# Optimization experiments

Measured on AMD Instinct MI355X. Metric: run time of the kernel, lower is better.

## Reference

```python
import jax, jax.numpy as jnp
import numpy as np

B, N, F, G, H = 8, 1024, 512, 128, 8
D = F // H  # head_dim = 64


def setup_inputs() -> dict:
    key = jax.random.key(0)
    ks = jax.random.split(key, 24)
    def lin(k, fan_in, shape):
        return jax.random.normal(k, shape, jnp.float32) / np.sqrt(fan_in)
    return {
        "features": jax.random.normal(ks[0], (B, N, F), jnp.float32),
        "geometry": jax.random.normal(ks[1], (B, N, G), jnp.float32),
        "coords": jax.random.normal(ks[2], (B, N, 3), jnp.float32),
        # nnx.MultiHeadAttention params (q/k/v/out dense, with bias)
        "wq": lin(ks[3], F, (F, F)), "bq": jnp.zeros((F,), jnp.float32),
        "wk": lin(ks[4], F, (F, F)), "bk": jnp.zeros((F,), jnp.float32),
        "wv": lin(ks[5], F, (F, F)), "bv": jnp.zeros((F,), jnp.float32),
        "wo": lin(ks[6], F, (F, F)), "bo": jnp.zeros((F,), jnp.float32),
        # geometry q/k/v linears
        "gq_w": lin(ks[7], G, (G, F)), "gq_b": jnp.zeros((F,), jnp.float32),
        "gk_w": lin(ks[8], G, (G, F)), "gk_b": jnp.zeros((F,), jnp.float32),
        "gv_w": lin(ks[9], G, (G, F)), "gv_b": jnp.zeros((F,), jnp.float32),
        # distance MLP: Linear(1->H), gelu, Linear(H->H)
        "d1_w": lin(ks[10], 1, (1, H)), "d1_b": jnp.zeros((H,), jnp.float32),
        "d2_w": lin(ks[11], H, (H, H)), "d2_b": jnp.zeros((H,), jnp.float32),
        # output projection
        "op_w": lin(ks[12], F, (F, F)), "op_b": jnp.zeros((F,), jnp.float32),
    }


def _forward(features, geometry, coords,
             wq, bq, wk, bk, wv, bv, wo, bo,
             gq_w, gq_b, gk_w, gk_b, gv_w, gv_b,
             d1_w, d1_b, d2_w, d2_b, op_w, op_b):
    scale = jnp.sqrt(jnp.float32(D))
    # --- standard multi-head self-attention branch (nnx.MultiHeadAttention) ---
    q = (features @ wq + bq).reshape(B, N, H, D)
    k = (features @ wk + bk).reshape(B, N, H, D)
    v = (features @ wv + bv).reshape(B, N, H, D)
    scores = jnp.einsum("bqhd,bkhd->bhqk", q, k) / scale
    attn = jax.nn.softmax(scores, axis=-1)
    feat_att = jnp.einsum("bhqk,bkhd->bqhd", attn, v).reshape(B, N, F)
    feat_att = feat_att @ wo + bo
    # --- geometry attention branch ---
    gq = geometry @ gq_w + gq_b
    gk = geometry @ gk_w + gk_b
    gv = geometry @ gv_w + gv_b
    g_scores = jnp.einsum("bqd,bkd->bqk", gq, gk) / scale
    # pairwise distances (B,N,N,1); clamp for sqrt-at-zero safety (diagonal)
    diff = coords[:, :, None, :] - coords[:, None, :, :]
    dist = jnp.sqrt(jnp.maximum(jnp.sum(diff * diff, -1, keepdims=True), 1e-12))
    dw = jax.nn.gelu(dist @ d1_w + d1_b) @ d2_w + d2_b  # (B,N,N,H)
    # transpose to (B,H,N,N) then mean over heads == mean over last axis
    g_scores = g_scores + jnp.mean(dw, axis=-1)
    g_attn = jax.nn.softmax(g_scores, axis=-1)
    geom_att = jnp.einsum("bqk,bkd->bqd", g_attn, gv)
    return (feat_att + geom_att) @ op_w + op_b


def reference(features, geometry, coords,
              wq, bq, wk, bk, wv, bv, wo, bo,
              gq_w, gq_b, gk_w, gk_b, gv_w, gv_b,
              d1_w, d1_b, d2_w, d2_b, op_w, op_b):
    return _forward(features, geometry, coords,
                    wq, bq, wk, bk, wv, bv, wo, bo,
                    gq_w, gq_b, gk_w, gk_b, gv_w, gv_b,
                    d1_w, d1_b, d2_w, d2_b, op_w, op_b)
```

## Files before the change

kernel.cpp:

```cpp
#include <hip/hip_runtime.h>

typedef __bf16 bf16_t;
typedef __bf16 bf16x8 __attribute__((ext_vector_type(8)));
typedef __bf16 bf16x4v __attribute__((ext_vector_type(4)));
typedef float f32x4 __attribute__((ext_vector_type(4)));

#define MFMA16(a, b, c) __builtin_amdgcn_mfma_f32_16x16x32_bf16((a), (b), (c), 0, 0, 0)

static constexpr int B_ = 8, N_ = 1024, F_ = 512, H_ = 8;
static constexpr int M_ = B_ * N_;

__device__ __forceinline__ void gl_lds16(const bf16_t* gsrc, bf16_t* ldst) {
  __builtin_amdgcn_global_load_lds(
      (const __attribute__((address_space(1))) void*)gsrc,
      (__attribute__((address_space(3))) void*)ldst, 16, 0, 0);
}

__device__ __forceinline__ float gelu_tanh(float u) {
  float g = 0.7978845608028654f * fmaf(0.044715f * u * u, u, u);
  float e = __expf(2.f * g);
  float t = 1.f - 2.f / (e + 1.f);
  return 0.5f * u * (1.f + t);
}

struct PrepArgs {
  const float *features, *geometry;
  const float *wq, *wk, *wv, *wo, *op_w;
  const float *gq_w, *gk_w, *gv_w;
  const float *bq, *bk, *bv, *gq_b, *gk_b, *gv_b;
  const float *d1w, *d1b, *d2w, *d2b;
  bf16_t *featBF, *geomBF, *WqkvT, *GqkvT, *WoT, *OpT;
  float *bqkv, *gqkvb, *dlut;
};

static constexpr int PR_C0 = 4096;
static constexpr int PR_C1 = PR_C0 + 1024;
static constexpr int PR_WQ = PR_C1 + 256;
static constexpr int PR_WK = PR_WQ + 256;
static constexpr int PR_WV = PR_WK + 256;
static constexpr int PR_WO = PR_WV + 256;
static constexpr int PR_OP = PR_WO + 256;
static constexpr int PR_GQ = PR_OP + 64;
static constexpr int PR_GK = PR_GQ + 64;
static constexpr int PR_GV = PR_GK + 64;
static constexpr int PR_B1 = PR_GV + 6;
static constexpr int PR_B2 = PR_B1 + 6;
static constexpr int PR_LUT = PR_B2 + 16;
static constexpr int PR_TOTAL = PR_LUT;

__device__ __forceinline__ void prep_cast(const float* __restrict__ in,
                                          bf16_t* __restrict__ out, int blk) {
  int i = blk * 256 + threadIdx.x;
  float4 v = ((const float4*)in)[i];
  bf16x4v o;
  o[0] = (bf16_t)v.x; o[1] = (bf16_t)v.y; o[2] = (bf16_t)v.z; o[3] = (bf16_t)v.w;
  ((bf16x4v*)out)[i] = o;
}

__device__ __forceinline__ void prep_transpose(const float* __restrict__ W,
                                               bf16_t* __restrict__ Wt,
                                               int K, int N, int ldo, int idx,
                                               float (*t)[33]) {
  const int bx = idx & 15, by = idx >> 4;
  const int kb = by * 32, cb = bx * 32;
  const int tx = threadIdx.x & 31, ty = threadIdx.x >> 5;
#pragma unroll
  for (int i = 0; i < 4; ++i)
    t[ty * 4 + i][tx] = W[(long)(kb + ty * 4 + i) * N + cb + tx];
  __syncthreads();
#pragma unroll
  for (int i = 0; i < 4; ++i)
    Wt[(long)(cb + ty * 4 + i) * ldo + kb + tx] = (bf16_t)t[tx][ty * 4 + i];
}

__global__ __launch_bounds__(256) void k_prep(PrepArgs p) {
  __shared__ float tsh[32][33];
  const int blk = blockIdx.x;
  if (blk < PR_C0) {
    prep_cast(p.features, p.featBF, blk);
  } else if (blk < PR_C1) {
    prep_cast(p.geometry, p.geomBF, blk - PR_C0);
  } else if (blk < PR_WQ) {
    prep_transpose(p.wq, p.WqkvT, 512, 512, 512, blk - PR_C1, tsh);
  } else if (blk < PR_WK) {
    prep_transpose(p.wk, p.WqkvT + 512 * 512, 512, 512, 512, blk - PR_WQ, tsh);
  } else if (blk < PR_WV) {
    prep_transpose(p.wv, p.WqkvT + 1024 * 512, 512, 512, 512, blk - PR_WK, tsh);
  } else if (blk < PR_WO) {
    prep_transpose(p.wo, p.WoT, 512, 512, 512, blk - PR_WV, tsh);
  } else if (blk < PR_OP) {
    prep_transpose(p.op_w, p.OpT, 512, 512, 512, blk - PR_WO, tsh);
  } else if (blk < PR_GQ) {
    prep_transpose(p.gq_w, p.GqkvT, 128, 512, 128, blk - PR_OP, tsh);
  } else if (blk < PR_GK) {
    prep_transpose(p.gk_w, p.GqkvT + 512 * 128, 128, 512, 128, blk - PR_GQ, tsh);
  } else if (blk < PR_GV) {
    prep_transpose(p.gv_w, p.GqkvT + 1024 * 128, 128, 512, 128, blk - PR_GK, tsh);
  } else if (blk < PR_B1) {
    int i = (blk - PR_GV) * 256 + threadIdx.x;
    p.bqkv[i] = i < 512 ? p.bq[i] : (i < 1024 ? p.bk[i - 512] : p.bv[i - 1024]);
  } else if (blk < PR_B2) {
    int i = (blk - PR_B1) * 256 + threadIdx.x;
    p.gqkvb[i] = i < 512 ? p.gq_b[i] : (i < 1024 ? p.gk_b[i - 512] : p.gv_b[i - 1024]);
  } else {
    int i = (blk - PR_B2) * 256 + threadIdx.x;
    float d = (i + 0.5f) * (16.f / 4096.f);
    float s = 0.f;
#pragma unroll
    for (int h = 0; h < 8; ++h) s += p.d2b[h];
    s *= 0.125f;
#pragma unroll
    for (int j = 0; j < 8; ++j) {
      float w2 = 0.f;
#pragma unroll
      for (int h = 0; h < 8; ++h) w2 += p.d2w[j * 8 + h];
      s = fmaf(gelu_tanh(fmaf(d, p.d1w[j], p.d1b[j])), w2 * 0.125f, s);
    }
    p.dlut[i] = s;
  }
}

__global__ void k_transpose_v2(const bf16_t* __restrict__ QKV,
                               const bf16_t* __restrict__ GQKV,
                               bf16_t* __restrict__ Vt, bf16_t* __restrict__ GVt) {
  __shared__ bf16_t t[32][33];
  const int z = blockIdx.z;
  const bf16_t* in = z < 8 ? QKV : GQKV;
  bf16_t* out = z < 8 ? Vt : GVt;
  const int b = z & 7;
  const int cb = blockIdx.x * 32, nb = blockIdx.y * 32;
  const int tx = threadIdx.x, ty = threadIdx.y;
#pragma unroll
  for (int i = 0; i < 4; ++i)
    t[ty * 4 + i][tx] = in[((long)b * 1024 + nb + ty * 4 + i) * 1536 + 1024 + cb + tx];
  __syncthreads();
#pragma unroll
  for (int i = 0; i < 4; ++i)
    out[((long)b * 512 + cb + ty * 4 + i) * 1024 + nb + tx] = t[tx][ty * 4 + i];
}

struct GemmArgs {
  const bf16_t* A; const bf16_t* Bt;
  const float* bias; const float* addSrc;
  const float* coords; const float* lut;
  float* outF; bf16_t* outB;
  long strideAb; long strideBb;
  int lda, ldb, K, ldout;
  float scale;
};

__device__ __forceinline__ void gemm128_core(const GemmArgs& g, int mBase, int cBase,
                                             bf16_t (*As)[64], bf16_t (*Bs)[64]) {
  const int tid = threadIdx.x;
  const int w = tid >> 6, lane = tid & 63;
  const int lr = lane & 15, lg = lane >> 4;
  const int wr = w >> 1, wc = w & 1;
  const int batch = mBase >> 10;

  const int srow = lane >> 3;
  const int scol = (lane & 7) * 8;
  const bf16_t* Ag = g.A + (long)batch * g.strideAb +
                     (long)((mBase & 1023) + w * 32 + srow) * g.lda + scol;
  const bf16_t* Bg = g.Bt + (long)batch * g.strideBb +
                     (long)(cBase + w * 32 + srow) * g.ldb + scol;
  bf16_t* Al = &As[w * 32][0];
  bf16_t* Bl = &Bs[w * 32][0];

  f32x4 zero = {0.f, 0.f, 0.f, 0.f};
  f32x4 acc[4][4];
#pragma unroll
  for (int i = 0; i < 4; ++i)
#pragma unroll
    for (int j = 0; j < 4; ++j) acc[i][j] = zero;

  for (int k0 = 0; k0 < g.K; k0 += 64) {
#pragma unroll
    for (int is = 0; is < 4; ++is) {
      gl_lds16(Ag + (long)(is * 8) * g.lda + k0, Al + is * 8 * 64);
      gl_lds16(Bg + (long)(is * 8) * g.ldb + k0, Bl + is * 8 * 64);
    }
    __syncthreads();
#pragma unroll
    for (int ks = 0; ks < 2; ++ks) {
      bf16x8 a[4], b[4];
#pragma unroll
      for (int i = 0; i < 4; ++i) {
        a[i] = *(const bf16x8*)(&As[wr * 64 + i * 16 + lr][ks * 32 + lg * 8]);
        b[i] = *(const bf16x8*)(&Bs[wc * 64 + i * 16 + lr][ks * 32 + lg * 8]);
      }
#pragma unroll
      for (int mf = 0; mf < 4; ++mf)
#pragma unroll
        for (int nf = 0; nf < 4; ++nf)
          acc[mf][nf] = MFMA16(a[mf], b[nf], acc[mf][nf]);
    }
    __syncthreads();
  }

  const int c0 = cBase + wc * 64;
  float bias4[4];
#pragma unroll
  for (int nf = 0; nf < 4; ++nf)
    bias4[nf] = g.bias ? g.bias[c0 + nf * 16 + lr] : 0.f;
#pragma unroll
  for (int mf = 0; mf < 4; ++mf) {
    const int r0 = mBase + wr * 64 + mf * 16 + lg * 4;
#pragma unroll
    for (int nf = 0; nf < 4; ++nf) {
      const int c = c0 + nf * 16 + lr;
#pragma unroll
      for (int rg = 0; rg < 4; ++rg) {
        const int r = r0 + rg;
        float v = acc[mf][nf][rg] * g.scale + bias4[nf];
        if (g.addSrc) v += g.addSrc[(long)r * g.ldout + c];
        const long oi = (long)r * g.ldout + c;
        if (g.outF) g.outF[oi] = v;
        if (g.outB) g.outB[oi] = (bf16_t)v;
      }
    }
  }
}

__global__ __launch_bounds__(256) void k_gemm128_dual(GemmArgs g1, GemmArgs g2) {
  __shared__ alignas(16) bf16_t As[128][64];
  __shared__ alignas(16) bf16_t Bs[128][64];
  const int y = blockIdx.y;
  if (y < 64) gemm128_core(g1, y * 128, blockIdx.x * 128, As, Bs);
  else        gemm128_core(g2, (y - 64) * 128, blockIdx.x * 128, As, Bs);
}

__device__ __forceinline__ void gemm128_dist(const GemmArgs& g, int mBase, int cBase,
                                             char* smemc) {
  bf16_t (*As)[64] = (bf16_t (*)[64])smemc;
  bf16_t (*Bs)[64] = (bf16_t (*)[64])(smemc + 16384);
  bf16_t* Lut = (bf16_t*)(smemc + 32768);
  const int tid = threadIdx.x;
  const int w = tid >> 6, lane = tid & 63;
  const int lr = lane & 15, lg = lane >> 4;
  const int wr = w >> 1, wc = w & 1;
  const int batch = mBase >> 10;

  {
    const float4* src = (const float4*)g.lut;
#pragma unroll
    for (int i = 0; i < 4; ++i) {
      float4 v = src[tid + i * 256];
      bf16x4v o;
      o[0] = (bf16_t)v.x; o[1] = (bf16_t)v.y; o[2] = (bf16_t)v.z; o[3] = (bf16_t)v.w;
      ((bf16x4v*)Lut)[tid + i * 256] = o;
    }
  }

  const int srow = lane >> 3;
  const int scol = (lane & 7) * 8;
  const bf16_t* Ag = g.A + (long)batch * g.strideAb +
                     (long)((mBase & 1023) + w * 32 + srow) * g.lda + scol;
  const bf16_t* Bg = g.Bt + (long)batch * g.strideBb +
                     (long)(cBase + w * 32 + srow) * g.ldb + scol;
  bf16_t* Al = &As[w * 32][0];
  bf16_t* Bl = &Bs[w * 32][0];

  f32x4 zero = {0.f, 0.f, 0.f, 0.f};
  f32x4 acc[4][4];
#pragma unroll
  for (int i = 0; i < 4; ++i)
#pragma unroll
    for (int j = 0; j < 4; ++j) acc[i][j] = zero;

  for (int k0 = 0; k0 < g.K; k0 += 64) {
#pragma unroll
    for (int is = 0; is < 4; ++is) {
      gl_lds16(Ag + (long)(is * 8) * g.lda + k0, Al + is * 8 * 64);
      gl_lds16(Bg + (long)(is * 8) * g.ldb + k0, Bl + is * 8 * 64);
    }
    __syncthreads();
#pragma unroll
    for (int ks = 0; ks < 2; ++ks) {
      bf16x8 a[4], b[4];
#pragma unroll
      for (int i = 0; i < 4; ++i) {
        a[i] = *(const bf16x8*)(&As[wr * 64 + i * 16 + lr][ks * 32 + lg * 8]);
        b[i] = *(const bf16x8*)(&Bs[wc * 64 + i * 16 + lr][ks * 32 + lg * 8]);
      }
#pragma unroll
      for (int mf = 0; mf < 4; ++mf)
#pragma unroll
        for (int nf = 0; nf < 4; ++nf)
          acc[mf][nf] = MFMA16(a[mf], b[nf], acc[mf][nf]);
    }
    __syncthreads();
  }

  const int c0 = cBase + wc * 64;
  float ckx[4], cky[4], ckz[4];
#pragma unroll
  for (int nf = 0; nf < 4; ++nf) {
    const float* ck = g.coords + ((long)batch * 1024 + c0 + nf * 16 + lr) * 3;
    ckx[nf] = ck[0]; cky[nf] = ck[1]; ckz[nf] = ck[2];
  }
#pragma unroll
  for (int mf = 0; mf < 4; ++mf) {
    const int r0 = mBase + wr * 64 + mf * 16 + lg * 4;
    float cqx[4], cqy[4], cqz[4];
#pragma unroll
    for (int rg = 0; rg < 4; ++rg) {
      const float* cq = g.coords + ((long)batch * 1024 + ((r0 + rg) & 1023)) * 3;
      cqx[rg] = cq[0]; cqy[rg] = cq[1]; cqz[rg] = cq[2];
    }
#pragma unroll
    for (int nf = 0; nf < 4; ++nf) {
      const int c = c0 + nf * 16 + lr;
#pragma unroll
      for (int rg = 0; rg < 4; ++rg) {
        const int r = r0 + rg;
        float v = acc[mf][nf][rg] * g.scale;
        float dx = cqx[rg] - ckx[nf], dy = cqy[rg] - cky[nf], dz = cqz[rg] - ckz[nf];
        float d = sqrtf(fmaxf(dx * dx + dy * dy + dz * dz, 1e-12f));
        int idx = (int)(d * 256.f);
        idx = idx > 4095 ? 4095 : idx;
        v += (float)Lut[idx];
        g.outF[(long)r * g.ldout + c] = v;
      }
    }
  }
}

__device__ __forceinline__ void flash_core(const bf16_t* __restrict__ QKV,
                                           const bf16_t* __restrict__ Vt,
                                           bf16_t* __restrict__ fatt,
                                           int qx, int bh, char* smemc) {
  bf16_t (*Ks)[64][64] = (bf16_t (*)[64][64])smemc;
  bf16_t (*Vs)[64][64] = (bf16_t (*)[64][64])(smemc + 16384);
  char* Plb = smemc + 32768;
  const int wave = threadIdx.x >> 6, lane = threadIdx.x & 63;
  const int lr = lane & 15, lg = (lane >> 4) & 3;
  const int b = bh >> 3, h = bh & 7;
  const int qbase = qx * 64 + wave * 16;

  const bf16_t* Qb = QKV + (long)b * 1024 * 1536 + h * 64;
  const bf16_t* Kb = Qb + 512;
  const bf16_t* Vg = Vt + ((long)b * 512 + h * 64) * 1024;

  constexpr float SCL = 0.18033688011112042f;
  bf16x8 q_[2];
#pragma unroll
  for (int dh = 0; dh < 2; ++dh) {
    bf16x8 raw = *(const bf16x8*)(Qb + (long)(qbase + lr) * 1536 + dh * 32 + lg * 8);
#pragma unroll
    for (int j = 0; j < 8; ++j) q_[dh][j] = (bf16_t)((float)raw[j] * SCL);
  }

  const int srow = lane >> 3;
  const int scol = (((lane & 7) ^ srow) << 3);
  const bf16_t* KgB = Kb + (long)(wave * 16 + srow) * 1536 + scol;
  const bf16_t* VgB = Vg + (long)(wave * 16 + srow) * 1024 + scol;

  auto stage = [&](int buf, int kt) {
#pragma unroll
    for (int i = 0; i < 2; ++i) {
      gl_lds16(KgB + (long)(kt + i * 8) * 1536, &Ks[buf][wave * 16 + i * 8][0]);
      gl_lds16(VgB + (long)(i * 8) * 1024 + kt, &Vs[buf][wave * 16 + i * 8][0]);
    }
  };

  f32x4 zero = {0.f, 0.f, 0.f, 0.f};
  f32x4 oacc[4] = {zero, zero, zero, zero};
  float lsum0 = 0.f, lsum1 = 0.f;
  const int swz = (lr & 7) << 4;
  char* PlW = Plb + wave * 1280;

  stage(0, 0);
  asm volatile("s_waitcnt vmcnt(0)" ::: "memory");
  __syncthreads();

  auto tile = [&](const int buf, int t) __attribute__((always_inline)) {
    if (t < 15) stage(buf ^ 1, (t + 1) * 64);
    const char* KB = (const char*)&Ks[buf][0][0];
    const char* VB = (const char*)&Vs[buf][0][0];
#pragma unroll
    for (int kk = 0; kk < 2; ++kk) {
      f32x4 S[2];
      __builtin_amdgcn_s_setprio(1);
#pragma unroll
      for (int kh = 0; kh < 2; ++kh) {
        const int row = kk * 32 + kh * 16 + lr;
        bf16x8 k0 = *(const bf16x8*)(KB + row * 128 + ((lg * 16) ^ swz));
        bf16x8 k1 = *(const bf16x8*)(KB + row * 128 + ((64 + lg * 16) ^ swz));
        f32x4 tt = MFMA16(k0, q_[0], zero);
        S[kh] = MFMA16(k1, q_[1], tt);
      }
      __builtin_amdgcn_s_setprio(0);
#pragma unroll
      for (int kh = 0; kh < 2; ++kh) {
        bf16x4v pp;
#pragma unroll
        for (int r = 0; r < 4; ++r) {
          float e = exp2f(S[kh][r]);
          if (kh) lsum1 += e; else lsum0 += e;
          pp[r] = (bf16_t)e;
        }
        *(bf16x4v*)(PlW + lr * 80 + kh * 32 + lg * 8) = pp;
      }
      asm volatile("s_waitcnt lgkmcnt(0)" ::: "memory");
      const bf16x8 pa = *(const bf16x8*)(PlW + lr * 80 + lg * 16);
      __builtin_amdgcn_s_setprio(1);
#pragma unroll
      for (int ct = 0; ct < 4; ++ct) {
        const int vrow = ct * 16 + lr;
        bf16x8 vf = *(const bf16x8*)(VB + vrow * 128 + ((kk * 64 + lg * 16) ^ swz));
        oacc[ct] = MFMA16(pa, vf, oacc[ct]);
      }
      __builtin_amdgcn_s_setprio(0);
    }
    asm volatile("s_waitcnt vmcnt(0)" ::: "memory");
    __syncthreads();
  };

  for (int tt = 0; tt < 8; ++tt) {
    tile(0, tt * 2);
    tile(1, tt * 2 + 1);
  }

  float lsum = lsum0 + lsum1;
  lsum += __shfl_xor(lsum, 16);
  lsum += __shfl_xor(lsum, 32);
#pragma unroll
  for (int r = 0; r < 4; ++r) {
    float inv = 1.f / __shfl(lsum, lg * 4 + r, 64);
    int q = qbase + lg * 4 + r;
    bf16_t* orow = fatt + ((long)b * 1024 + q) * 512 + h * 64;
#pragma unroll
    for (int ct = 0; ct < 4; ++ct)
      orow[ct * 16 + lr] = (bf16_t)(oacc[ct][r] * inv);
  }
}

__global__ __launch_bounds__(256) void k_gsc_flash(GemmArgs g,
                                                   const bf16_t* __restrict__ QKV,
                                                   const bf16_t* __restrict__ Vt,
                                                   bf16_t* __restrict__ fatt) {
  __shared__ alignas(16) char smem[40960];
  const int bx = blockIdx.x;
  if (bx < 1024) {
    flash_core(QKV, Vt, fatt, bx & 15, bx >> 4, smem);
  } else {
    const int i = bx - 1024;
    gemm128_dist(g, (i >> 3) * 128, (i & 7) * 128, smem);
  }
}

__device__ __forceinline__ void gemm_n64_core(const GemmArgs& g, int mBase, int cBase,
                                              char* smemc) {
  bf16_t (*As)[64] = (bf16_t (*)[64])smemc;
  bf16_t (*Bs)[64] = (bf16_t (*)[64])(smemc + 16384);
  const int tid = threadIdx.x;
  const int w = tid >> 6, lane = tid & 63;
  const int lr = lane & 15, lg = lane >> 4;
  const int wr = w >> 1, wc = w & 1;
  const int batch = mBase >> 10;

  const int srow = lane >> 3;
  const int scol = (lane & 7) * 8;
  const bf16_t* Ag = g.A + (long)batch * g.strideAb +
                     (long)((mBase & 1023) + w * 32 + srow) * g.lda + scol;
  const bf16_t* Bg = g.Bt + (long)batch * g.strideBb +
                     (long)(cBase + w * 16 + srow) * g.ldb + scol;
  bf16_t* Al = &As[w * 32][0];
  bf16_t* Bl = &Bs[w * 16][0];

  f32x4 zero = {0.f, 0.f, 0.f, 0.f};
  f32x4 acc[4][2];
#pragma unroll
  for (int i = 0; i < 4; ++i)
#pragma unroll
    for (int j = 0; j < 2; ++j) acc[i][j] = zero;

  for (int k0 = 0; k0 < g.K; k0 += 64) {
#pragma unroll
    for (int is = 0; is < 4; ++is)
      gl_lds16(Ag + (long)(is * 8) * g.lda + k0, Al + is * 8 * 64);
#pragma unroll
    for (int is = 0; is < 2; ++is)
      gl_lds16(Bg + (long)(is * 8) * g.ldb + k0, Bl + is * 8 * 64);
    __syncthreads();
#pragma unroll
    for (int ks = 0; ks < 2; ++ks) {
      bf16x8 a[4], b[2];
#pragma unroll
      for (int i = 0; i < 4; ++i)
        a[i] = *(const bf16x8*)(&As[wr * 64 + i * 16 + lr][ks * 32 + lg * 8]);
#pragma unroll
      for (int j = 0; j < 2; ++j)
        b[j] = *(const bf16x8*)(&Bs[wc * 32 + j * 16 + lr][ks * 32 + lg * 8]);
#pragma unroll
      for (int mf = 0; mf < 4; ++mf)
#pragma unroll
        for (int nf = 0; nf < 2; ++nf)
          acc[mf][nf] = MFMA16(a[mf], b[nf], acc[mf][nf]);
    }
    __syncthreads();
  }

  const int c0 = cBase + wc * 32;
  float bias2[2];
#pragma unroll
  for (int nf = 0; nf < 2; ++nf)
    bias2[nf] = g.bias ? g.bias[c0 + nf * 16 + lr] : 0.f;
#pragma unroll
  for (int mf = 0; mf < 4; ++mf) {
    const int r0 = mBase + wr * 64 + mf * 16 + lg * 4;
#pragma unroll
    for (int nf = 0; nf < 2; ++nf) {
      const int c = c0 + nf * 16 + lr;
#pragma unroll
      for (int rg = 0; rg < 4; ++rg) {
        const int r = r0 + rg;
        float v = acc[mf][nf][rg] * g.scale + bias2[nf];
        if (g.addSrc) v += g.addSrc[(long)r * g.ldout + c];
        const long oi = (long)r * g.ldout + c;
        if (g.outF) g.outF[oi] = v;
        if (g.outB) g.outB[oi] = (bf16_t)v;
      }
    }
  }
}

__global__ __launch_bounds__(256) void k_gemm_n64(GemmArgs g) {
  __shared__ alignas(16) char smem[24576];
  gemm_n64_core(g, blockIdx.y * 128, blockIdx.x * 64, smem);
}

__device__ __forceinline__ void softmax_core(const float* __restrict__ S,
                                             bf16_t* __restrict__ P, int row,
                                             float* redM, float* redS) {
  const float* s = S + (long)row * 1024;
  const int tid = threadIdx.x;
  float4 v = ((const float4*)s)[tid];
  float mx = fmaxf(fmaxf(v.x, v.y), fmaxf(v.z, v.w));
#pragma unroll
  for (int d = 1; d < 64; d <<= 1) mx = fmaxf(mx, __shfl_xor(mx, d));
  if ((tid & 63) == 0) redM[tid >> 6] = mx;
  __syncthreads();
  mx = fmaxf(fmaxf(redM[0], redM[1]), fmaxf(redM[2], redM[3]));
  float e0 = __expf(v.x - mx), e1 = __expf(v.y - mx);
  float e2 = __expf(v.z - mx), e3 = __expf(v.w - mx);
  float sm = e0 + e1 + e2 + e3;
#pragma unroll
  for (int d = 1; d < 64; d <<= 1) sm += __shfl_xor(sm, d);
  if ((tid & 63) == 0) redS[tid >> 6] = sm;
  __syncthreads();
  sm = redS[0] + redS[1] + redS[2] + redS[3];
  float inv = 1.f / sm;
  bf16x4v o;
  o[0] = (bf16_t)(e0 * inv); o[1] = (bf16_t)(e1 * inv);
  o[2] = (bf16_t)(e2 * inv); o[3] = (bf16_t)(e3 * inv);
  ((bf16x4v*)(P + (long)row * 1024))[tid] = o;
}

__global__ __launch_bounds__(256) void k_sm_combf(GemmArgs g,
                                                  const float* __restrict__ S,
                                                  bf16_t* __restrict__ P) {
  __shared__ alignas(16) char smem[24576];
  __shared__ float redM[4], redS[4];
  const int bx = blockIdx.x;
  if (bx < 512) {
    gemm_n64_core(g, (bx >> 3) * 128, (bx & 7) * 64, smem);
  } else {
    softmax_core(S, P, bx - 512, redM, redS);
  }
}

extern "C" void kernel_launch(void* const* d_in, const int* in_sizes, int n_in,
                              void* d_out, int out_size, void* d_ws, size_t ws_size,
                              hipStream_t stream) {
  const float* features = (const float*)d_in[0];
  const float* geometry = (const float*)d_in[1];
  const float* coords   = (const float*)d_in[2];
  const float* wq = (const float*)d_in[3];  const float* bq = (const float*)d_in[4];
  const float* wk = (const float*)d_in[5];  const float* bk = (const float*)d_in[6];
  const float* wv = (const float*)d_in[7];  const float* bv = (const float*)d_in[8];
  const float* wo = (const float*)d_in[9];  const float* bo = (const float*)d_in[10];
  const float* gq_w = (const float*)d_in[11]; const float* gq_b = (const float*)d_in[12];
  const float* gk_w = (const float*)d_in[13]; const float* gk_b = (const float*)d_in[14];
  const float* gv_w = (const float*)d_in[15]; const float* gv_b = (const float*)d_in[16];
  const float* d1_w = (const float*)d_in[17]; const float* d1_b = (const float*)d_in[18];
  const float* d2_w = (const float*)d_in[19]; const float* d2_b = (const float*)d_in[20];
  const float* op_w = (const float*)d_in[21]; const float* op_b = (const float*)d_in[22];

  size_t off = 0;
  auto carve = [&](size_t bytes) {
    void* p = (char*)d_ws + off;
    off += (bytes + 255) & ~(size_t)255;
    return p;
  };
  bf16_t* featBF = (bf16_t*)carve((size_t)M_ * F_ * 2);
  bf16_t* geomBF = (bf16_t*)carve((size_t)M_ * 128 * 2);
  bf16_t* WqkvT  = (bf16_t*)carve((size_t)1536 * 512 * 2);
  bf16_t* GqkvT  = (bf16_t*)carve((size_t)1536 * 128 * 2);
  bf16_t* WoT    = (bf16_t*)carve((size_t)512 * 512 * 2);
  bf16_t* OpT    = (bf16_t*)carve((size_t)512 * 512 * 2);
  float*  bqkv   = (float*)carve(1536 * 4);
  float*  gqkvb  = (float*)carve(1536 * 4);
  float*  dlut   = (float*)carve(4096 * 4);
  bf16_t* QKV    = (bf16_t*)carve((size_t)M_ * 1536 * 2);
  bf16_t* GQKV   = (bf16_t*)carve((size_t)M_ * 1536 * 2);
  bf16_t* Vt     = (bf16_t*)carve((size_t)B_ * 512 * 1024 * 2);
  bf16_t* GVt    = (bf16_t*)carve((size_t)B_ * 512 * 1024 * 2);
  float*  gsc    = (float*)carve((size_t)M_ * 1024 * 4);
  bf16_t* gattn  = (bf16_t*)carve((size_t)M_ * 1024 * 2);
  bf16_t* fatt   = (bf16_t*)carve((size_t)M_ * 512 * 2);
  float*  combF  = (float*)carve((size_t)M_ * 512 * 4);
  bf16_t* combB  = (bf16_t*)carve((size_t)M_ * 512 * 2);
  if (off > ws_size) return;

  PrepArgs p;
  p.features = features; p.geometry = geometry;
  p.wq = wq; p.wk = wk; p.wv = wv; p.wo = wo; p.op_w = op_w;
  p.gq_w = gq_w; p.gk_w = gk_w; p.gv_w = gv_w;
  p.bq = bq; p.bk = bk; p.bv = bv; p.gq_b = gq_b; p.gk_b = gk_b; p.gv_b = gv_b;
  p.d1w = d1_w; p.d1b = d1_b; p.d2w = d2_w; p.d2b = d2_b;
  p.featBF = featBF; p.geomBF = geomBF; p.WqkvT = WqkvT; p.GqkvT = GqkvT;
  p.WoT = WoT; p.OpT = OpT; p.bqkv = bqkv; p.gqkvb = gqkvb; p.dlut = dlut;
  k_prep<<<PR_TOTAL, 256, 0, stream>>>(p);

  auto mk = [](const bf16_t* A, long sAb, int lda, const bf16_t* Bt, long sBb, int ldb,
               int K, const float* bias, const float* addSrc, float* outF, bf16_t* outB,
               int ldout, float scale, const float* coords, const float* lut) {
    GemmArgs g;
    g.A = A; g.Bt = Bt; g.bias = bias; g.addSrc = addSrc;
    g.coords = coords; g.lut = lut; g.outF = outF; g.outB = outB;
    g.strideAb = sAb; g.strideBb = sBb; g.lda = lda; g.ldb = ldb;
    g.K = K; g.ldout = ldout; g.scale = scale;
    return g;
  };

  k_gemm128_dual<<<dim3(12, 128), 256, 0, stream>>>(
      mk(featBF, (long)1024 * 512, 512, WqkvT, 0, 512, 512,
         bqkv, nullptr, nullptr, QKV, 1536, 1.f, nullptr, nullptr),
      mk(geomBF, (long)1024 * 128, 128, GqkvT, 0, 128, 128,
         gqkvb, nullptr, nullptr, GQKV, 1536, 1.f, nullptr, nullptr));
  k_transpose_v2<<<dim3(16, 32, 16), dim3(32, 8), 0, stream>>>(QKV, GQKV, Vt, GVt);
  k_gsc_flash<<<1536, 256, 0, stream>>>(
      mk(GQKV, (long)1024 * 1536, 1536, GQKV + 512, (long)1024 * 1536, 1536, 512,
         nullptr, nullptr, gsc, nullptr, 1024, 0.125f, coords, dlut),
      QKV, Vt, fatt);
  k_sm_combf<<<8704, 256, 0, stream>>>(
      mk(fatt, (long)1024 * 512, 512, WoT, 0, 512, 512,
         bo, nullptr, combF, nullptr, 512, 1.f, nullptr, nullptr),
      gsc, gattn);
  k_gemm_n64<<<dim3(8, 64), 256, 0, stream>>>(
      mk(gattn, (long)1024 * 1024, 1024, GVt, (long)512 * 1024, 1024, 1024,
         nullptr, combF, nullptr, combB, 512, 1.f, nullptr, nullptr));
  k_gemm_n64<<<dim3(8, 64), 256, 0, stream>>>(
      mk(combB, (long)1024 * 512, 512, OpT, 0, 512, 512,
         op_b, nullptr, (float*)d_out, nullptr, 512, 1.f, nullptr, nullptr));
}
```

Before: 196.3 us.

## Fuse geometry softmax exp into score GEMM and normalize rows in PV GEMM

The geometry score kernel now applies exp2 (with log2e folded into scale and the distance LUT) and writes unnormalized bf16 probabilities instead of fp32 scores, eliminating the separate softmax kernel and its fp32 read/write traffic. Row sums are computed in the following P·V GEMM via an extra MFMA against a ones vector and applied as a per-row reciprocal in the epilogue. The flash attention kernel similarly replaces scalar lsum accumulation plus shuffles with an MFMA against ones. Dropping the max subtraction risks overflow for large logits, and bf16 row sums accumulate from rounded probabilities.

```diff
diff --git a/kernel.cpp b/kernel.cpp
--- a/kernel.cpp
+++ b/kernel.cpp
@@ -9,6 +9,7 @@
 
 static constexpr int B_ = 8, N_ = 1024, F_ = 512, H_ = 8;
 static constexpr int M_ = B_ * N_;
+static constexpr float LOG2E = 1.4426950408889634f;
 
 __device__ __forceinline__ void gl_lds16(const bf16_t* gsrc, bf16_t* ldst) {
   __builtin_amdgcn_global_load_lds(
@@ -246,7 +247,8 @@
     for (int i = 0; i < 4; ++i) {
       float4 v = src[tid + i * 256];
       bf16x4v o;
-      o[0] = (bf16_t)v.x; o[1] = (bf16_t)v.y; o[2] = (bf16_t)v.z; o[3] = (bf16_t)v.w;
+      o[0] = (bf16_t)(v.x * LOG2E); o[1] = (bf16_t)(v.y * LOG2E);
+      o[2] = (bf16_t)(v.z * LOG2E); o[3] = (bf16_t)(v.w * LOG2E);
       ((bf16x4v*)Lut)[tid + i * 256] = o;
     }
   }
@@ -318,8 +320,7 @@
         float d = sqrtf(fmaxf(dx * dx + dy * dy + dz * dz, 1e-12f));
         int idx = (int)(d * 256.f);
         idx = idx > 4095 ? 4095 : idx;
-        v += (float)Lut[idx];
-        g.outF[(long)r * g.ldout + c] = v;
+        g.outB[(long)r * g.ldout + c] = (bf16_t)exp2f(v + (float)Lut[idx]);
       }
     }
   }
@@ -349,6 +350,9 @@
 #pragma unroll
     for (int j = 0; j < 8; ++j) q_[dh][j] = (bf16_t)((float)raw[j] * SCL);
   }
+  bf16x8 onesb;
+#pragma unroll
+  for (int j = 0; j < 8; ++j) onesb[j] = (bf16_t)1.0f;
 
   const int srow = lane >> 3;
   const int scol = (((lane & 7) ^ srow) << 3);
@@ -365,7 +369,7 @@
 
   f32x4 zero = {0.f, 0.f, 0.f, 0.f};
   f32x4 oacc[4] = {zero, zero, zero, zero};
-  float lsum0 = 0.f, lsum1 = 0.f;
+  f32x4 oL = zero;
   const int swz = (lr & 7) << 4;
   char* PlW = Plb + wave * 1280;
 
@@ -394,11 +398,7 @@
       for (int kh = 0; kh < 2; ++kh) {
         bf16x4v pp;
 #pragma unroll
-        for (int r = 0; r < 4; ++r) {
-          float e = exp2f(S[kh][r]);
-          if (kh) lsum1 += e; else lsum0 += e;
-          pp[r] = (bf16_t)e;
-        }
+        for (int r = 0; r < 4; ++r) pp[r] = (bf16_t)exp2f(S[kh][r]);
         *(bf16x4v*)(PlW + lr * 80 + kh * 32 + lg * 8) = pp;
       }
       asm volatile("s_waitcnt lgkmcnt(0)" ::: "memory");
@@ -410,6 +410,7 @@
         bf16x8 vf = *(const bf16x8*)(VB + vrow * 128 + ((kk * 64 + lg * 16) ^ swz));
         oacc[ct] = MFMA16(pa, vf, oacc[ct]);
       }
+      oL = MFMA16(pa, onesb, oL);
       __builtin_amdgcn_s_setprio(0);
     }
     asm volatile("s_waitcnt vmcnt(0)" ::: "memory");
@@ -421,12 +422,9 @@
     tile(1, tt * 2 + 1);
   }
 
-  float lsum = lsum0 + lsum1;
-  lsum += __shfl_xor(lsum, 16);
-  lsum += __shfl_xor(lsum, 32);
 #pragma unroll
   for (int r = 0; r < 4; ++r) {
-    float inv = 1.f / __shfl(lsum, lg * 4 + r, 64);
+    float inv = 1.f / oL[r];
     int q = qbase + lg * 4 + r;
     bf16_t* orow = fatt + ((long)b * 1024 + q) * 512 + h * 64;
 #pragma unroll
@@ -449,14 +447,15 @@
   }
 }
 
-__device__ __forceinline__ void gemm_n64_core(const GemmArgs& g, int mBase, int cBase,
-                                              char* smemc) {
-  bf16_t (*As)[64] = (bf16_t (*)[64])smemc;
-  bf16_t (*Bs)[64] = (bf16_t (*)[64])(smemc + 16384);
+template <int RSUM>
+__global__ __launch_bounds__(256) void k_gemm_n64(GemmArgs g) {
+  __shared__ alignas(16) bf16_t As[128][64];
+  __shared__ alignas(16) bf16_t Bs[64][64];
   const int tid = threadIdx.x;
   const int w = tid >> 6, lane = tid & 63;
   const int lr = lane & 15, lg = lane >> 4;
   const int wr = w >> 1, wc = w & 1;
+  const int mBase = blockIdx.y * 128, cBase = blockIdx.x * 64;
   const int batch = mBase >> 10;
 
   const int srow = lane >> 3;
@@ -474,6 +473,10 @@
   for (int i = 0; i < 4; ++i)
 #pragma unroll
     for (int j = 0; j < 2; ++j) acc[i][j] = zero;
+  f32x4 lacc[4] = {zero, zero, zero, zero};
+  bf16x8 onesb;
+#pragma unroll
+  for (int j = 0; j < 8; ++j) onesb[j] = (bf16_t)1.0f;
 
   for (int k0 = 0; k0 < g.K; k0 += 64) {
 #pragma unroll
@@ -497,6 +500,11 @@
 #pragma unroll
         for (int nf = 0; nf < 2; ++nf)
           acc[mf][nf] = MFMA16(a[mf], b[nf], acc[mf][nf]);
+      if constexpr (RSUM) {
+#pragma unroll
+        for (int mf = 0; mf < 4; ++mf)
+          lacc[mf] = MFMA16(a[mf], onesb, lacc[mf]);
+      }
     }
     __syncthreads();
   }
@@ -509,6 +517,11 @@
 #pragma unroll
   for (int mf = 0; mf < 4; ++mf) {
     const int r0 = mBase + wr * 64 + mf * 16 + lg * 4;
+    float linv[4];
+    if constexpr (RSUM) {
+#pragma unroll
+      for (int rg = 0; rg < 4; ++rg) linv[rg] = 1.f / lacc[mf][rg];
+    }
 #pragma unroll
     for (int nf = 0; nf < 2; ++nf) {
       const int c = c0 + nf * 16 + lr;
@@ -516,57 +529,13 @@
       for (int rg = 0; rg < 4; ++rg) {
         const int r = r0 + rg;
         float v = acc[mf][nf][rg] * g.scale + bias2[nf];
+        if constexpr (RSUM) v *= linv[rg];
         if (g.addSrc) v += g.addSrc[(long)r * g.ldout + c];
         const long oi = (long)r * g.ldout + c;
         if (g.outF) g.outF[oi] = v;
         if (g.outB) g.outB[oi] = (bf16_t)v;
       }
     }
-  }
-}
-
-__global__ __launch_bounds__(256) void k_gemm_n64(GemmArgs g) {
-  __shared__ alignas(16) char smem[24576];
-  gemm_n64_core(g, blockIdx.y * 128, blockIdx.x * 64, smem);
-}
-
-__device__ __forceinline__ void softmax_core(const float* __restrict__ S,
-                                             bf16_t* __restrict__ P, int row,
-                                             float* redM, float* redS) {
-  const float* s = S + (long)row * 1024;
-  const int tid = threadIdx.x;
-  float4 v = ((const float4*)s)[tid];
-  float mx = fmaxf(fmaxf(v.x, v.y), fmaxf(v.z, v.w));
-#pragma unroll
-  for (int d = 1; d < 64; d <<= 1) mx = fmaxf(mx, __shfl_xor(mx, d));
-  if ((tid & 63) == 0) redM[tid >> 6] = mx;
-  __syncthreads();
-  mx = fmaxf(fmaxf(redM[0], redM[1]), fmaxf(redM[2], redM[3]));
-  float e0 = __expf(v.x - mx), e1 = __expf(v.y - mx);
-  float e2 = __expf(v.z - mx), e3 = __expf(v.w - mx);
-  float sm = e0 + e1 + e2 + e3;
-#pragma unroll
-  for (int d = 1; d < 64; d <<= 1) sm += __shfl_xor(sm, d);
-  if ((tid & 63) == 0) redS[tid >> 6] = sm;
-  __syncthreads();
-  sm = redS[0] + redS[1] + redS[2] + redS[3];
-  float inv = 1.f / sm;
-  bf16x4v o;
-  o[0] = (bf16_t)(e0 * inv); o[1] = (bf16_t)(e1 * inv);
-  o[2] = (bf16_t)(e2 * inv); o[3] = (bf16_t)(e3 * inv);
-  ((bf16x4v*)(P + (long)row * 1024))[tid] = o;
-}
-
-__global__ __launch_bounds__(256) void k_sm_combf(GemmArgs g,
-                                                  const float* __restrict__ S,
-                                                  bf16_t* __restrict__ P) {
-  __shared__ alignas(16) char smem[24576];
-  __shared__ float redM[4], redS[4];
-  const int bx = blockIdx.x;
-  if (bx < 512) {
-    gemm_n64_core(g, (bx >> 3) * 128, (bx & 7) * 64, smem);
-  } else {
-    softmax_core(S, P, bx - 512, redM, redS);
   }
 }
 
@@ -606,8 +575,7 @@
   bf16_t* GQKV   = (bf16_t*)carve((size_t)M_ * 1536 * 2);
   bf16_t* Vt     = (bf16_t*)carve((size_t)B_ * 512 * 1024 * 2);
   bf16_t* GVt    = (bf16_t*)carve((size_t)B_ * 512 * 1024 * 2);
-  float*  gsc    = (float*)carve((size_t)M_ * 1024 * 4);
-  bf16_t* gattn  = (bf16_t*)carve((size_t)M_ * 1024 * 2);
+  bf16_t* Pun    = (bf16_t*)carve((size_t)M_ * 1024 * 2);
   bf16_t* fatt   = (bf16_t*)carve((size_t)M_ * 512 * 2);
   float*  combF  = (float*)carve((size_t)M_ * 512 * 4);
   bf16_t* combB  = (bf16_t*)carve((size_t)M_ * 512 * 2);
@@ -642,16 +610,15 @@
   k_transpose_v2<<<dim3(16, 32, 16), dim3(32, 8), 0, stream>>>(QKV, GQKV, Vt, GVt);
   k_gsc_flash<<<1536, 256, 0, stream>>>(
       mk(GQKV, (long)1024 * 1536, 1536, GQKV + 512, (long)1024 * 1536, 1536, 512,
-         nullptr, nullptr, gsc, nullptr, 1024, 0.125f, coords, dlut),
+         nullptr, nullptr, nullptr, Pun, 1024, 0.125f * LOG2E, coords, dlut),
       QKV, Vt, fatt);
-  k_sm_combf<<<8704, 256, 0, stream>>>(
+  k_gemm_n64<0><<<dim3(8, 64), 256, 0, stream>>>(
       mk(fatt, (long)1024 * 512, 512, WoT, 0, 512, 512,
-         bo, nullptr, combF, nullptr, 512, 1.f, nullptr, nullptr),
-      gsc, gattn);
-  k_gemm_n64<<<dim3(8, 64), 256, 0, stream>>>(
-      mk(gattn, (long)1024 * 1024, 1024, GVt, (long)512 * 1024, 1024, 1024,
+         bo, nullptr, combF, nullptr, 512, 1.f, nullptr, nullptr));
+  k_gemm_n64<1><<<dim3(8, 64), 256, 0, stream>>>(
+      mk(Pun, (long)1024 * 1024, 1024, GVt, (long)512 * 1024, 1024, 1024,
          nullptr, combF, nullptr, combB, 512, 1.f, nullptr, nullptr));
-  k_gemm_n64<<<dim3(8, 64), 256, 0, stream>>>(
+  k_gemm_n64<0><<<dim3(8, 64), 256, 0, stream>>>(
       mk(combB, (long)1024 * 512, 512, OpT, 0, 512, 512,
          op_b, nullptr, (float*)d_out, nullptr, 512, 1.f, nullptr, nullptr));
 }
```

Result: faster. 187.8 us (-4.3%).
